# Kernel tuning notes

Measured on AMD Instinct MI355X. Metric: run time of the kernel, lower is better.

The kernel has to match this reference:

```python
import jax, jax.numpy as jnp
import numpy as np

DIM = 1024
Q_HEADS = 16
KV_HEADS = 4
DIM_HEAD = DIM // Q_HEADS  # 64
SOFTCLAMP = 50.0
EPS = 1e-8


def rotate_half(x):
    x_even = x[..., ::2]
    x_odd = x[..., 1::2]
    return jnp.stack([-x_odd, x_even], axis=-1).reshape(x.shape)


def setup_inputs() -> dict:
    key = jax.random.key(0)
    ks = jax.random.split(key, 10)
    B, S = 1, 2048
    dim_q = DIM_HEAD * Q_HEADS   # 1024
    dim_kv = DIM_HEAD * KV_HEADS  # 256
    std = 0.02
    x = jax.random.normal(ks[0], (B, S, DIM), dtype=jnp.float32)
    positions = jnp.broadcast_to(jnp.arange(S, dtype=jnp.int32)[None, :], (B, S))
    # causal mask: True = disallowed (torch semantics: allowed = ~attn_mask)
    attn_mask = jnp.triu(jnp.ones((S, S), dtype=bool), k=1)
    return {
        "x": x,
        "positions": positions,
        "attn_mask": attn_mask,
        "Wq": jax.random.normal(ks[1], (DIM, dim_q), jnp.float32) * std,
        "Wk": jax.random.normal(ks[2], (DIM, dim_kv), jnp.float32) * std,
        "Wv": jax.random.normal(ks[3], (DIM, dim_kv), jnp.float32) * std,
        "Wo": jax.random.normal(ks[4], (dim_q, DIM), jnp.float32) * std,
        "Wg": jax.random.normal(ks[5], (DIM, Q_HEADS), jnp.float32) * std,
        "Wm": jax.random.normal(ks[6], (DIM, KV_HEADS), jnp.float32) * std,
        "bm": jnp.zeros((KV_HEADS,), jnp.float32),
        "Wvr": jax.random.normal(ks[7], (DIM, dim_kv), jnp.float32) * std,
        "k_scale": jnp.ones((KV_HEADS, DIM_HEAD), jnp.float32),
    }


def reference(x, positions, attn_mask, Wq, Wk, Wv, Wo, Wg, Wm, bm, Wvr, k_scale):
    b, s, _ = x.shape
    h, qh, dh = KV_HEADS, Q_HEADS, DIM_HEAD
    g = qh // h

    q = (x @ Wq).reshape(b, s, qh, dh).transpose(0, 2, 1, 3)  # [b,qh,s,dh]
    k = (x @ Wk).reshape(b, s, h, dh).transpose(0, 2, 1, 3)   # [b,h,s,dh]
    v = (x @ Wv).reshape(b, s, h, dh).transpose(0, 2, 1, 3)

    # value-residual gating: v = lerp(v, residual_v, mix)
    residual_v = (x @ Wvr).reshape(b, s, h, dh).transpose(0, 2, 1, 3)
    mix = jax.nn.sigmoid(x @ Wm + bm).transpose(0, 2, 1)[..., None]  # [b,h,s,1]
    v = v + mix * (residual_v - v)

    # multi-head RMSNorm on k
    rms = jnp.sqrt(jnp.mean(k * k, axis=-1, keepdims=True) + EPS)
    k = k / rms * k_scale[None, :, None, :]

    # rotary embeddings (identical for all heads -> broadcast over head dim)
    inv_freq = 1.0 / (10000.0 ** (jnp.arange(0, dh, 2, dtype=jnp.float32) / dh))
    freqs = positions.astype(jnp.float32)[..., None] * inv_freq  # [b,s,dh/2]
    cos = jnp.repeat(jnp.cos(freqs), 2, axis=-1)[:, None, :, :]  # [b,1,s,dh]
    sin = jnp.repeat(jnp.sin(freqs), 2, axis=-1)[:, None, :, :]
    q = q * cos + rotate_half(q) * sin
    k = k * cos + rotate_half(k) * sin

    # grouped-query attention with softclamped scores
    scale = dh ** -0.5
    qg = q.reshape(b, h, g, s, dh)
    sim = jnp.einsum('bhgqd,bhkd->bhgqk', qg, k) * scale
    sim = jnp.tanh(sim / SOFTCLAMP) * SOFTCLAMP
    allowed = ~attn_mask  # [s,s]
    sim = jnp.where(allowed[None, None, None, :, :], sim, jnp.finfo(sim.dtype).min)
    attn = jax.nn.softmax(sim, axis=-1)
    out = jnp.einsum('bhgqk,bhkd->bhgqd', attn, v).reshape(b, qh, s, dh)

    # per-query-head sigmoid gates
    gates = jax.nn.sigmoid(x @ Wg).transpose(0, 2, 1)[..., None]  # [b,qh,s,1]
    out = out * gates

    out = out.transpose(0, 2, 1, 3).reshape(b, s, qh * dh)
    return out @ Wo
```

## Files before the change

### kernel.cpp

```cpp
#include <hip/hip_runtime.h>
#include <hip/hip_bf16.h>
#include <math.h>

typedef unsigned short u16;
typedef unsigned int u32;
typedef __attribute__((ext_vector_type(8))) __bf16 bf16x8;
typedef __attribute__((ext_vector_type(4))) float f32x4;

__device__ inline u16 f2bf(float f) {
  u32 b = __float_as_uint(f);
  b += 0x7FFFu + ((b >> 16) & 1u);
  return (u16)(b >> 16);
}
__device__ inline float bf2f(u16 b) { return __uint_as_float((u32)b << 16); }

__device__ __forceinline__ void gll16(const void* gp, void* lp) {
  __builtin_amdgcn_global_load_lds(
      (const __attribute__((address_space(1))) void*)gp,
      (__attribute__((address_space(3))) void*)lp, 16, 0, 0);
}

__global__ __launch_bounds__(256) void prep_all_k(
    const float* __restrict__ x, const int* __restrict__ positions,
    const float* __restrict__ Wq, const float* __restrict__ Wk,
    const float* __restrict__ Wv, const float* __restrict__ Wvr,
    const float* __restrict__ Wo, const float* __restrict__ Wg,
    const float* __restrict__ Wm, u16* __restrict__ xb,
    u16* __restrict__ WallT, u16* __restrict__ WoT, float* __restrict__ rtab) {
  __shared__ float tile[32][33];
  int bid = blockIdx.x, tid = threadIdx.x;
  if (bid < 1024) {
    int i = (bid * 256 + tid) * 8;
    float4 v0 = *(const float4*)&x[i];
    float4 v1 = *(const float4*)&x[i + 4];
    uint4 pk;
    pk.x = (u32)f2bf(v0.x) | ((u32)f2bf(v0.y) << 16);
    pk.y = (u32)f2bf(v0.z) | ((u32)f2bf(v0.w) << 16);
    pk.z = (u32)f2bf(v1.x) | ((u32)f2bf(v1.y) << 16);
    pk.w = (u32)f2bf(v1.z) | ((u32)f2bf(v1.w) << 16);
    *(uint4*)&xb[i] = pk;
    return;
  }
  if (bid >= 3968) {
    int idx = (bid - 3968) * 256 + tid;
    int s = idx >> 5, f = idx & 31;
    float inv = __expf(-(float)f * (9.210340371976184f / 32.f));
    float ang = (float)positions[s] * inv;
    rtab[(size_t)s * 64 + f] = cosf(ang);
    rtab[(size_t)s * 64 + 32 + f] = sinf(ang);
    return;
  }
  int b2 = bid - 1024;
  int k0 = (b2 & 31) * 32;
  int ybl = b2 >> 5;
  int tx = tid & 31, ty = tid >> 5;
  const float* src;
  int scol, sN, drow;
  u16* dst;
  if (ybl >= 60) {
    src = Wo; scol = (ybl - 60) * 32; sN = 1024; dst = WoT; drow = scol;
  } else {
    int n0 = ybl * 32;
    if (n0 >= 1792) {
#pragma unroll
      for (int j = 0; j < 4; ++j) {
        int n = n0 + ty * 4 + j, j2 = n - 1792, k = k0 + tx;
        float val = (j2 < 16) ? Wg[(size_t)k * 16 + j2]
                  : (j2 < 20) ? Wm[(size_t)k * 4 + (j2 - 16)] : 0.f;
        WallT[(size_t)n * 1024 + k] = f2bf(val);
      }
      return;
    }
    dst = WallT; drow = n0;
    if (n0 < 1024) { src = Wq; scol = n0; sN = 1024; }
    else if (n0 < 1280) { src = Wk; scol = n0 - 1024; sN = 256; }
    else if (n0 < 1536) { src = Wv; scol = n0 - 1280; sN = 256; }
    else { src = Wvr; scol = n0 - 1536; sN = 256; }
  }
#pragma unroll
  for (int j = 0; j < 4; ++j)
    tile[ty * 4 + j][tx] = src[(size_t)(k0 + ty * 4 + j) * sN + scol + tx];
  __syncthreads();
#pragma unroll
  for (int j = 0; j < 4; ++j)
    dst[(size_t)(drow + ty * 4 + j) * 1024 + k0 + tx] = f2bf(tile[tx][ty * 4 + j]);
}

template <int BM, bool BF16_OUT>
__global__ __launch_bounds__(512) void gemm_bf16_k(
    const u16* __restrict__ A, const u16* __restrict__ Bt, void* __restrict__ Cv,
    int M, int N, int K) {
  constexpr int MI = BM / 32;
  __shared__ __align__(16) u16 As[BM * 64];
  __shared__ __align__(16) u16 Bs[128 * 64];
  int tid = threadIdx.x;
  int w = tid >> 6, l = tid & 63;
  int wr = w >> 2, wc = w & 3;
  int lr = l & 15, lg = l >> 4;
  int lrow = l >> 3, lcol = (l & 7) * 8;
  int m0 = blockIdx.y * BM, n0 = blockIdx.x * 128;
  f32x4 zero = {0.f, 0.f, 0.f, 0.f};
  f32x4 acc[MI][2];
#pragma unroll
  for (int mi = 0; mi < MI; ++mi)
#pragma unroll
    for (int ni = 0; ni < 2; ++ni) acc[mi][ni] = zero;

  for (int kt = 0; kt < K; kt += 64) {
    __syncthreads();
#pragma unroll
    for (int t = 0; t < BM / 64; ++t) {
      int seg = t * 8 + w;
      gll16(&A[(size_t)(m0 + seg * 8 + lrow) * K + kt + lcol], &As[seg * 512]);
    }
#pragma unroll
    for (int t = 0; t < 2; ++t) {
      int seg = t * 8 + w;
      gll16(&Bt[(size_t)(n0 + seg * 8 + lrow) * K + kt + lcol], &Bs[seg * 512]);
    }
    __syncthreads();
#pragma unroll
    for (int kw = 0; kw < 2; ++kw) {
      bf16x8 af[MI], bfr[2];
#pragma unroll
      for (int mi = 0; mi < MI; ++mi)
        af[mi] = *(const bf16x8*)&As[(wr * (BM / 2) + mi * 16 + lr) * 64 + kw * 32 + lg * 8];
#pragma unroll
      for (int ni = 0; ni < 2; ++ni)
        bfr[ni] = *(const bf16x8*)&Bs[(wc * 32 + ni * 16 + lr) * 64 + kw * 32 + lg * 8];
#pragma unroll
      for (int mi = 0; mi < MI; ++mi)
#pragma unroll
        for (int ni = 0; ni < 2; ++ni)
          acc[mi][ni] = __builtin_amdgcn_mfma_f32_16x16x32_bf16(
              af[mi], bfr[ni], acc[mi][ni], 0, 0, 0);
    }
  }
#pragma unroll
  for (int mi = 0; mi < MI; ++mi)
#pragma unroll
    for (int ni = 0; ni < 2; ++ni)
#pragma unroll
      for (int r = 0; r < 4; ++r) {
        int row = m0 + wr * (BM / 2) + mi * 16 + lg * 4 + r;
        int col = n0 + wc * 32 + ni * 16 + lr;
        if (BF16_OUT)
          ((u16*)Cv)[(size_t)row * N + col] = f2bf(acc[mi][ni][r]);
        else
          ((float*)Cv)[(size_t)row * N + col] = acc[mi][ni][r];
      }
}

__global__ __launch_bounds__(256) void postproc_k(
    const float* __restrict__ bm, const float* __restrict__ ksc,
    const float* __restrict__ rtab, u16* __restrict__ qkvrb,
    u16* __restrict__ kb, u16* __restrict__ vb, float* __restrict__ g_out) {
  int s = blockIdx.x, tid = threadIdx.x;
  int lane = tid & 63, w = tid >> 6;
  u16* row = qkvrb + (size_t)s * 1920;
  const float* tr = rtab + (size_t)s * 64;
  if (tid < 16)
    g_out[s * 16 + tid] = 1.f / (1.f + __expf(-bf2f(row[1792 + tid])));
  int h = w, d = lane;
  float c = tr[d >> 1], sn = tr[32 + (d >> 1)];
  {
    float mixv = 1.f / (1.f + __expf(-(bf2f(row[1808 + h]) + bm[h])));
    float vv = bf2f(row[1280 + h * 64 + d]);
    float rv = bf2f(row[1536 + h * 64 + d]);
    vb[((size_t)h * 2048 + s) * 64 + d] = f2bf(vv + mixv * (rv - vv));
  }
  {
    float kv = bf2f(row[1024 + h * 64 + d]);
    float ss = kv * kv;
#pragma unroll
    for (int off = 32; off > 0; off >>= 1) ss += __shfl_xor(ss, off);
    float rms = sqrtf(ss * (1.f / 64.f) + 1e-8f);
    float kn = kv / rms * ksc[h * 64 + d];
    float partner = __shfl_xor(kn, 1);
    kb[((size_t)h * 2048 + s) * 64 + d] =
        f2bf((d & 1) ? fmaf(kn, c, partner * sn) : fmaf(kn, c, -partner * sn));
  }
#pragma unroll
  for (int r = 0; r < 4; ++r) {
    int e = r * 256 + tid;
    int dq = e & 63;
    float cq = tr[dq >> 1], sq = tr[32 + (dq >> 1)];
    float qv = bf2f(row[e]);
    float partner = __shfl_xor(qv, 1);
    float qr = (e & 1) ? fmaf(qv, cq, partner * sq) : fmaf(qv, cq, -partner * sq);
    row[e] = f2bf(qr * 0.125f);
  }
}

#define TPAD 66
__global__ __launch_bounds__(256) void vtrans_k(const u16* __restrict__ vb,
                                               u16* __restrict__ vtb) {
  __shared__ u16 tile[64 * TPAD];
  int h = blockIdx.y, s0 = blockIdx.x * 64;
  int t = threadIdx.x;
  {
    int r = t >> 2, cb = (t & 3) * 16;
    const u16* src = vb + ((size_t)h * 2048 + s0 + r) * 64 + cb;
    *(uint4*)&tile[r * TPAD + cb] = *(const uint4*)src;
    *(uint4*)&tile[r * TPAD + cb + 8] = *(const uint4*)(src + 8);
  }
  __syncthreads();
  int d = t >> 2, sb = (t & 3) * 16;
  u16 vals[16];
#pragma unroll
  for (int j = 0; j < 16; ++j) vals[j] = tile[(sb + j) * TPAD + d];
  uint4 a, b;
  a.x = (u32)vals[0] | ((u32)vals[1] << 16);
  a.y = (u32)vals[2] | ((u32)vals[3] << 16);
  a.z = (u32)vals[4] | ((u32)vals[5] << 16);
  a.w = (u32)vals[6] | ((u32)vals[7] << 16);
  b.x = (u32)vals[8] | ((u32)vals[9] << 16);
  b.y = (u32)vals[10] | ((u32)vals[11] << 16);
  b.z = (u32)vals[12] | ((u32)vals[13] << 16);
  b.w = (u32)vals[14] | ((u32)vals[15] << 16);
  u16* dst = vtb + ((size_t)h * 64 + d) * 2048 + s0 + sb;
  *(uint4*)dst = a;
  *(uint4*)(dst + 8) = b;
}

#define KPAD 72
__global__ __launch_bounds__(512) void attn_k(
    const u16* __restrict__ qkvrb, const u16* __restrict__ kb,
    const u16* __restrict__ vtb, const float* __restrict__ g,
    u16* __restrict__ aob) {
  __shared__ __align__(16) u16 smem[36864];
  int head = blockIdx.x, hkv = head >> 2;
  int tid = threadIdx.x;
  int w = tid >> 6, l = tid & 63;
  int grp = w >> 2, wi = w & 3;
  int lr = l & 15, lg = l >> 4;
  int gtid = wi * 64 + l;
  int skey = gtid >> 2, sdb = (gtid & 3) * 16;
  u16* KsBase = smem + grp * 18432;
  float* mbuf = (float*)smem;
  f32x4 zero = {0.f, 0.f, 0.f, 0.f};
  const float C1 = 0.057707801635558534f;
  const float C2 = -144.26950408889634f;
  int src_a = lr + (lg & 1) * 32, src_b = src_a + 16;
  bool hi = (lg & 2) != 0;
#pragma unroll 1
  for (int half = 0; half < 2; ++half) {
    int rb = half ? (int)blockIdx.y : (31 - (int)blockIdx.y);
    int row0 = rb * 64;
    const u16* qrow = qkvrb + (size_t)(row0 + wi * 16 + lr) * 1920 + head * 64;
    bf16x8 qf0 = *(const bf16x8*)&qrow[lg * 8];
    bf16x8 qf1 = *(const bf16x8*)&qrow[32 + lg * 8];
    f32x4 acc_o[4];
#pragma unroll
    for (int nd = 0; nd < 4; ++nd) acc_o[nd] = zero;
    float l_part = 0.f;
    int qglob = row0 + wi * 16 + lr;
    int c = grp;
    uint4 rk0, rk1, rv0, rv1;
    if (c <= rb) {
      const u16* kp = kb + ((size_t)hkv * 2048 + c * 64 + skey) * 64 + sdb;
      rk0 = *(const uint4*)kp;
      rk1 = *(const uint4*)(kp + 8);
      const u16* vp = vtb + ((size_t)(hkv * 64 + skey)) * 2048 + c * 64 + sdb;
      rv0 = *(const uint4*)vp;
      rv1 = *(const uint4*)(vp + 8);
      *(uint4*)&KsBase[skey * KPAD + sdb] = rk0;
      *(uint4*)&KsBase[skey * KPAD + sdb + 8] = rk1;
      *(uint4*)&KsBase[4608 + skey * KPAD + sdb] = rv0;
      *(uint4*)&KsBase[4608 + skey * KPAD + sdb + 8] = rv1;
    }
    __syncthreads();
    int nmax = (rb >> 1) + 1;
#pragma unroll 1
    for (int i = 0; i < nmax; ++i, c += 2) {
      bool valid = (c <= rb);
      bool nvalid = (c + 2 <= rb);
      if (nvalid) {
        int nb = (c + 2) * 64;
        const u16* kp = kb + ((size_t)hkv * 2048 + nb + skey) * 64 + sdb;
        rk0 = *(const uint4*)kp;
        rk1 = *(const uint4*)(kp + 8);
        const u16* vp = vtb + ((size_t)(hkv * 64 + skey)) * 2048 + nb + sdb;
        rv0 = *(const uint4*)vp;
        rv1 = *(const uint4*)(vp + 8);
      }
      if (valid) {
        u16* Ks = KsBase + (i & 1) * 9216;
        u16* Vt = Ks + 4608;
        int kbase = c * 64;
        __builtin_amdgcn_s_setprio(1);
        f32x4 sa[4];
#pragma unroll
        for (int ni = 0; ni < 4; ++ni) {
          bf16x8 a0 = *(const bf16x8*)&Ks[(ni * 16 + lr) * KPAD + lg * 8];
          bf16x8 a1 = *(const bf16x8*)&Ks[(ni * 16 + lr) * KPAD + 32 + lg * 8];
          f32x4 t = __builtin_amdgcn_mfma_f32_16x16x32_bf16(a0, qf0, zero, 0, 0, 0);
          sa[ni] = __builtin_amdgcn_mfma_f32_16x16x32_bf16(a1, qf1, t, 0, 0, 0);
        }
        bool diag = (c == rb);
        u32 pkw[4][2];
#pragma unroll
        for (int ni = 0; ni < 4; ++ni) {
          float pv[4];
#pragma unroll
          for (int r = 0; r < 4; ++r) {
            float sv = sa[ni][r];
            float e = __builtin_amdgcn_exp2f(sv * C1);
            float p = __builtin_amdgcn_exp2f(C2 * __builtin_amdgcn_rcpf(e + 1.f));
            if (diag && (kbase + ni * 16 + lg * 4 + r) > qglob) p = 0.f;
            pv[r] = p;
            l_part += p;
          }
          asm("v_cvt_pk_bf16_f32 %0, %1, %2" : "=v"(pkw[ni][0]) : "v"(pv[0]), "v"(pv[1]));
          asm("v_cvt_pk_bf16_f32 %0, %1, %2" : "=v"(pkw[ni][1]) : "v"(pv[2]), "v"(pv[3]));
        }
        union { u32 w[4]; bf16x8 v; } pf0, pf1;
        {
          u32 t0[4], t1[4], t2[4], t3[4];
#define GATHER(T, NI)                          \
          T[0] = __shfl((int)pkw[NI][0], src_a);   \
          T[1] = __shfl((int)pkw[NI][1], src_a);   \
          T[2] = __shfl((int)pkw[NI][0], src_b);   \
          T[3] = __shfl((int)pkw[NI][1], src_b);
          GATHER(t0, 0)
          GATHER(t1, 1)
          GATHER(t2, 2)
          GATHER(t3, 3)
#undef GATHER
#pragma unroll
          for (int kq = 0; kq < 4; ++kq) {
            pf0.w[kq] = hi ? t1[kq] : t0[kq];
            pf1.w[kq] = hi ? t3[kq] : t2[kq];
          }
        }
#pragma unroll
        for (int nd = 0; nd < 4; ++nd) {
          bf16x8 v0 = *(const bf16x8*)&Vt[(nd * 16 + lr) * KPAD + lg * 8];
          bf16x8 v1 = *(const bf16x8*)&Vt[(nd * 16 + lr) * KPAD + 32 + lg * 8];
          acc_o[nd] = __builtin_amdgcn_mfma_f32_16x16x32_bf16(pf0.v, v0, acc_o[nd], 0, 0, 0);
          acc_o[nd] = __builtin_amdgcn_mfma_f32_16x16x32_bf16(pf1.v, v1, acc_o[nd], 0, 0, 0);
        }
        __builtin_amdgcn_s_setprio(0);
      }
      if (nvalid) {
        u16* Ksn = KsBase + ((i & 1) ^ 1) * 9216;
        *(uint4*)&Ksn[skey * KPAD + sdb] = rk0;
        *(uint4*)&Ksn[skey * KPAD + sdb + 8] = rk1;
        *(uint4*)&Ksn[4608 + skey * KPAD + sdb] = rv0;
        *(uint4*)&Ksn[4608 + skey * KPAD + sdb + 8] = rv1;
      }
      __syncthreads();
    }
    l_part += __shfl_xor(l_part, 16);
    l_part += __shfl_xor(l_part, 32);
    if (grp == 1) {
      float* mb = mbuf + (size_t)gtid * 17;
#pragma unroll
      for (int nd = 0; nd < 4; ++nd)
#pragma unroll
        for (int r = 0; r < 4; ++r) mb[nd * 4 + r] = acc_o[nd][r];
      mb[16] = l_part;
    }
    __syncthreads();
    if (grp == 0) {
      const float* mb = mbuf + (size_t)gtid * 17;
      float lt = l_part + mb[16];
#pragma unroll
      for (int r = 0; r < 4; ++r) {
        int row = row0 + wi * 16 + lg * 4 + r;
        float lv = __shfl(lt, lg * 4 + r);
        float sc = g[row * 16 + head] * __builtin_amdgcn_rcpf(lv);
#pragma unroll
        for (int nd = 0; nd < 4; ++nd)
          aob[(size_t)row * 1024 + head * 64 + nd * 16 + lr] =
              f2bf((acc_o[nd][r] + mb[nd * 4 + r]) * sc);
      }
    }
    __syncthreads();
  }
}

extern "C" void kernel_launch(void* const* d_in, const int* in_sizes, int n_in,
                              void* d_out, int out_size, void* d_ws,
                              size_t ws_size, hipStream_t stream) {
  const float* x = (const float*)d_in[0];
  const int* positions = (const int*)d_in[1];
  const float* Wq = (const float*)d_in[3];
  const float* Wk = (const float*)d_in[4];
  const float* Wv = (const float*)d_in[5];
  const float* Wo = (const float*)d_in[6];
  const float* Wg = (const float*)d_in[7];
  const float* Wm = (const float*)d_in[8];
  const float* bm = (const float*)d_in[9];
  const float* Wvr = (const float*)d_in[10];
  const float* ksc = (const float*)d_in[11];
  float* out = (float*)d_out;

  u16* xb = (u16*)d_ws;
  u16* WallT = xb + (size_t)2048 * 1024;
  u16* WoT = WallT + (size_t)1920 * 1024;
  u16* qkvrb = WoT + (size_t)1024 * 1024;
  u16* kbuf = qkvrb + (size_t)2048 * 1920;
  u16* vbuf = kbuf + (size_t)4 * 2048 * 64;
  u16* vtb = vbuf + (size_t)4 * 2048 * 64;
  float* gbuf = (float*)(vtb + (size_t)4 * 2048 * 64);
  float* rtab = gbuf + (size_t)2048 * 16;
  u16* aob = xb;

  prep_all_k<<<4224, 256, 0, stream>>>(x, positions, Wq, Wk, Wv, Wvr, Wo, Wg,
                                       Wm, xb, WallT, WoT, rtab);
  gemm_bf16_k<128, true><<<dim3(15, 16), 512, 0, stream>>>(xb, WallT, qkvrb,
                                                           2048, 1920, 1024);
  postproc_k<<<2048, 256, 0, stream>>>(bm, ksc, rtab, qkvrb, kbuf, vbuf, gbuf);
  vtrans_k<<<dim3(32, 4), 256, 0, stream>>>(vbuf, vtb);
  attn_k<<<dim3(16, 16), 512, 0, stream>>>(qkvrb, kbuf, vtb, gbuf, aob);
  gemm_bf16_k<64, false><<<dim3(8, 32), 512, 0, stream>>>(aob, WoT, out, 2048,
                                                          1024, 1024);
}
```

Before: 98.61 us.

## Drop LDS staging in attention, read K/V fragments directly from global

The attention kernel no longer stages K and V tiles through shared memory with double buffering and barriers. Each wave now loads its MFMA operand fragments straight from global memory and relies on the caches for reuse across waves. The grid goes from 256 blocks of 512 threads, each handling two row blocks with split-KV groups, to 512 blocks of 256 threads, each handling one row block. This removes the cross-group merge and all __syncthreads. The cost is redundant global/L2 traffic, since each of the 4 waves reloads the same K/V tile, and less latency hiding than the explicit prefetch gave.

Measured after the change: 134.4 us. 36.3% more time.

```diff
diff --git a/kernel.cpp b/kernel.cpp
--- a/kernel.cpp
+++ b/kernel.cpp
@@ -223,160 +223,102 @@
   *(uint4*)(dst + 8) = b;
 }
 
-#define KPAD 72
-__global__ __launch_bounds__(512) void attn_k(
+__global__ __launch_bounds__(256) void attn_k(
     const u16* __restrict__ qkvrb, const u16* __restrict__ kb,
     const u16* __restrict__ vtb, const float* __restrict__ g,
     u16* __restrict__ aob) {
-  __shared__ __align__(16) u16 smem[36864];
   int head = blockIdx.x, hkv = head >> 2;
+  int by = blockIdx.y;
+  int rb = (by < 16) ? (31 - by) : (by - 16);
+  int row0 = rb * 64;
   int tid = threadIdx.x;
-  int w = tid >> 6, l = tid & 63;
-  int grp = w >> 2, wi = w & 3;
+  int wi = tid >> 6, l = tid & 63;
   int lr = l & 15, lg = l >> 4;
-  int gtid = wi * 64 + l;
-  int skey = gtid >> 2, sdb = (gtid & 3) * 16;
-  u16* KsBase = smem + grp * 18432;
-  float* mbuf = (float*)smem;
   f32x4 zero = {0.f, 0.f, 0.f, 0.f};
   const float C1 = 0.057707801635558534f;
   const float C2 = -144.26950408889634f;
+  const u16* qrow = qkvrb + (size_t)(row0 + wi * 16 + lr) * 1920 + head * 64;
+  bf16x8 qf0 = *(const bf16x8*)&qrow[lg * 8];
+  bf16x8 qf1 = *(const bf16x8*)&qrow[32 + lg * 8];
+  f32x4 acc_o[4];
+#pragma unroll
+  for (int nd = 0; nd < 4; ++nd) acc_o[nd] = zero;
+  float l_part = 0.f;
+  int qglob = row0 + wi * 16 + lr;
   int src_a = lr + (lg & 1) * 32, src_b = src_a + 16;
   bool hi = (lg & 2) != 0;
+  const u16* kbase_p = kb + ((size_t)hkv * 2048 + lr) * 64 + lg * 8;
+  const u16* vbase_p = vtb + (size_t)(hkv * 64 + lr) * 2048 + lg * 8;
 #pragma unroll 1
-  for (int half = 0; half < 2; ++half) {
-    int rb = half ? (int)blockIdx.y : (31 - (int)blockIdx.y);
-    int row0 = rb * 64;
-    const u16* qrow = qkvrb + (size_t)(row0 + wi * 16 + lr) * 1920 + head * 64;
-    bf16x8 qf0 = *(const bf16x8*)&qrow[lg * 8];
-    bf16x8 qf1 = *(const bf16x8*)&qrow[32 + lg * 8];
-    f32x4 acc_o[4];
-#pragma unroll
-    for (int nd = 0; nd < 4; ++nd) acc_o[nd] = zero;
-    float l_part = 0.f;
-    int qglob = row0 + wi * 16 + lr;
-    int c = grp;
-    uint4 rk0, rk1, rv0, rv1;
-    if (c <= rb) {
-      const u16* kp = kb + ((size_t)hkv * 2048 + c * 64 + skey) * 64 + sdb;
-      rk0 = *(const uint4*)kp;
-      rk1 = *(const uint4*)(kp + 8);
-      const u16* vp = vtb + ((size_t)(hkv * 64 + skey)) * 2048 + c * 64 + sdb;
-      rv0 = *(const uint4*)vp;
-      rv1 = *(const uint4*)(vp + 8);
-      *(uint4*)&KsBase[skey * KPAD + sdb] = rk0;
-      *(uint4*)&KsBase[skey * KPAD + sdb + 8] = rk1;
-      *(uint4*)&KsBase[4608 + skey * KPAD + sdb] = rv0;
-      *(uint4*)&KsBase[4608 + skey * KPAD + sdb + 8] = rv1;
-    }
-    __syncthreads();
-    int nmax = (rb >> 1) + 1;
-#pragma unroll 1
-    for (int i = 0; i < nmax; ++i, c += 2) {
-      bool valid = (c <= rb);
-      bool nvalid = (c + 2 <= rb);
-      if (nvalid) {
-        int nb = (c + 2) * 64;
-        const u16* kp = kb + ((size_t)hkv * 2048 + nb + skey) * 64 + sdb;
-        rk0 = *(const uint4*)kp;
-        rk1 = *(const uint4*)(kp + 8);
-        const u16* vp = vtb + ((size_t)(hkv * 64 + skey)) * 2048 + nb + sdb;
-        rv0 = *(const uint4*)vp;
-        rv1 = *(const uint4*)(vp + 8);
+  for (int c = 0; c <= rb; ++c) {
+    int kb0 = c * 64;
+    __builtin_amdgcn_s_setprio(1);
+    f32x4 sa[4];
+#pragma unroll
+    for (int ni = 0; ni < 4; ++ni) {
+      const u16* kp = kbase_p + (size_t)(kb0 + ni * 16) * 64;
+      bf16x8 a0 = *(const bf16x8*)kp;
+      bf16x8 a1 = *(const bf16x8*)(kp + 32);
+      f32x4 t = __builtin_amdgcn_mfma_f32_16x16x32_bf16(a0, qf0, zero, 0, 0, 0);
+      sa[ni] = __builtin_amdgcn_mfma_f32_16x16x32_bf16(a1, qf1, t, 0, 0, 0);
+    }
+    bool diag = (c == rb);
+    u32 pkw[4][2];
+#pragma unroll
+    for (int ni = 0; ni < 4; ++ni) {
+      float pv[4];
+#pragma unroll
+      for (int r = 0; r < 4; ++r) {
+        float sv = sa[ni][r];
+        float e = __builtin_amdgcn_exp2f(sv * C1);
+        float p = __builtin_amdgcn_exp2f(C2 * __builtin_amdgcn_rcpf(e + 1.f));
+        if (diag && (kb0 + ni * 16 + lg * 4 + r) > qglob) p = 0.f;
+        pv[r] = p;
+        l_part += p;
       }
-      if (valid) {
-        u16* Ks = KsBase + (i & 1) * 9216;
-        u16* Vt = Ks + 4608;
-        int kbase = c * 64;
-        __builtin_amdgcn_s_setprio(1);
-        f32x4 sa[4];
-#pragma unroll
-        for (int ni = 0; ni < 4; ++ni) {
-          bf16x8 a0 = *(const bf16x8*)&Ks[(ni * 16 + lr) * KPAD + lg * 8];
-          bf16x8 a1 = *(const bf16x8*)&Ks[(ni * 16 + lr) * KPAD + 32 + lg * 8];
-          f32x4 t = __builtin_amdgcn_mfma_f32_16x16x32_bf16(a0, qf0, zero, 0, 0, 0);
-          sa[ni] = __builtin_amdgcn_mfma_f32_16x16x32_bf16(a1, qf1, t, 0, 0, 0);
-        }
-        bool diag = (c == rb);
-        u32 pkw[4][2];
-#pragma unroll
-        for (int ni = 0; ni < 4; ++ni) {
-          float pv[4];
-#pragma unroll
-          for (int r = 0; r < 4; ++r) {
-            float sv = sa[ni][r];
-            float e = __builtin_amdgcn_exp2f(sv * C1);
-            float p = __builtin_amdgcn_exp2f(C2 * __builtin_amdgcn_rcpf(e + 1.f));
-            if (diag && (kbase + ni * 16 + lg * 4 + r) > qglob) p = 0.f;
-            pv[r] = p;
-            l_part += p;
-          }
-          asm("v_cvt_pk_bf16_f32 %0, %1, %2" : "=v"(pkw[ni][0]) : "v"(pv[0]), "v"(pv[1]));
-          asm("v_cvt_pk_bf16_f32 %0, %1, %2" : "=v"(pkw[ni][1]) : "v"(pv[2]), "v"(pv[3]));
-        }
-        union { u32 w[4]; bf16x8 v; } pf0, pf1;
-        {
-          u32 t0[4], t1[4], t2[4], t3[4];
+      asm("v_cvt_pk_bf16_f32 %0, %1, %2" : "=v"(pkw[ni][0]) : "v"(pv[0]), "v"(pv[1]));
+      asm("v_cvt_pk_bf16_f32 %0, %1, %2" : "=v"(pkw[ni][1]) : "v"(pv[2]), "v"(pv[3]));
+    }
+    union { u32 w[4]; bf16x8 v; } pf0, pf1;
+    {
+      u32 t0[4], t1[4], t2[4], t3[4];
 #define GATHER(T, NI)                          \
-          T[0] = __shfl((int)pkw[NI][0], src_a);   \
-          T[1] = __shfl((int)pkw[NI][1], src_a);   \
-          T[2] = __shfl((int)pkw[NI][0], src_b);   \
-          T[3] = __shfl((int)pkw[NI][1], src_b);
-          GATHER(t0, 0)
-          GATHER(t1, 1)
-          GATHER(t2, 2)
-          GATHER(t3, 3)
+      T[0] = __shfl((int)pkw[NI][0], src_a);   \
+      T[1] = __shfl((int)pkw[NI][1], src_a);   \
+      T[2] = __shfl((int)pkw[NI][0], src_b);   \
+      T[3] = __shfl((int)pkw[NI][1], src_b);
+      GATHER(t0, 0)
+      GATHER(t1, 1)
+      GATHER(t2, 2)
+      GATHER(t3, 3)
 #undef GATHER
 #pragma unroll
-          for (int kq = 0; kq < 4; ++kq) {
-            pf0.w[kq] = hi ? t1[kq] : t0[kq];
-            pf1.w[kq] = hi ? t3[kq] : t2[kq];
-          }
-        }
-#pragma unroll
-        for (int nd = 0; nd < 4; ++nd) {
-          bf16x8 v0 = *(const bf16x8*)&Vt[(nd * 16 + lr) * KPAD + lg * 8];
-          bf16x8 v1 = *(const bf16x8*)&Vt[(nd * 16 + lr) * KPAD + 32 + lg * 8];
-          acc_o[nd] = __builtin_amdgcn_mfma_f32_16x16x32_bf16(pf0.v, v0, acc_o[nd], 0, 0, 0);
-          acc_o[nd] = __builtin_amdgcn_mfma_f32_16x16x32_bf16(pf1.v, v1, acc_o[nd], 0, 0, 0);
-        }
-        __builtin_amdgcn_s_setprio(0);
+      for (int kq = 0; kq < 4; ++kq) {
+        pf0.w[kq] = hi ? t1[kq] : t0[kq];
+        pf1.w[kq] = hi ? t3[kq] : t2[kq];
       }
-      if (nvalid) {
-        u16* Ksn = KsBase + ((i & 1) ^ 1) * 9216;
-        *(uint4*)&Ksn[skey * KPAD + sdb] = rk0;
-        *(uint4*)&Ksn[skey * KPAD + sdb + 8] = rk1;
-        *(uint4*)&Ksn[4608 + skey * KPAD + sdb] = rv0;
-        *(uint4*)&Ksn[4608 + skey * KPAD + sdb + 8] = rv1;
-      }
-      __syncthreads();
-    }
-    l_part += __shfl_xor(l_part, 16);
-    l_part += __shfl_xor(l_part, 32);
-    if (grp == 1) {
-      float* mb = mbuf + (size_t)gtid * 17;
-#pragma unroll
-      for (int nd = 0; nd < 4; ++nd)
-#pragma unroll
-        for (int r = 0; r < 4; ++r) mb[nd * 4 + r] = acc_o[nd][r];
-      mb[16] = l_part;
-    }
-    __syncthreads();
-    if (grp == 0) {
-      const float* mb = mbuf + (size_t)gtid * 17;
-      float lt = l_part + mb[16];
-#pragma unroll
-      for (int r = 0; r < 4; ++r) {
-        int row = row0 + wi * 16 + lg * 4 + r;
-        float lv = __shfl(lt, lg * 4 + r);
-        float sc = g[row * 16 + head] * __builtin_amdgcn_rcpf(lv);
-#pragma unroll
-        for (int nd = 0; nd < 4; ++nd)
-          aob[(size_t)row * 1024 + head * 64 + nd * 16 + lr] =
-              f2bf((acc_o[nd][r] + mb[nd * 4 + r]) * sc);
-      }
-    }
-    __syncthreads();
+    }
+#pragma unroll
+    for (int nd = 0; nd < 4; ++nd) {
+      const u16* vp = vbase_p + (size_t)nd * 16 * 2048 + kb0;
+      bf16x8 v0 = *(const bf16x8*)vp;
+      bf16x8 v1 = *(const bf16x8*)(vp + 32);
+      acc_o[nd] = __builtin_amdgcn_mfma_f32_16x16x32_bf16(pf0.v, v0, acc_o[nd], 0, 0, 0);
+      acc_o[nd] = __builtin_amdgcn_mfma_f32_16x16x32_bf16(pf1.v, v1, acc_o[nd], 0, 0, 0);
+    }
+    __builtin_amdgcn_s_setprio(0);
+  }
+  l_part += __shfl_xor(l_part, 16);
+  l_part += __shfl_xor(l_part, 32);
+#pragma unroll
+  for (int r = 0; r < 4; ++r) {
+    int row = row0 + wi * 16 + lg * 4 + r;
+    float lv = __shfl(l_part, lg * 4 + r);
+    float sc = g[row * 16 + head] * __builtin_amdgcn_rcpf(lv);
+#pragma unroll
+    for (int nd = 0; nd < 4; ++nd)
+      aob[(size_t)row * 1024 + head * 64 + nd * 16 + lr] =
+          f2bf(acc_o[nd][r] * sc);
   }
 }
 
@@ -413,7 +355,7 @@
                                                            2048, 1920, 1024);
   postproc_k<<<2048, 256, 0, stream>>>(bm, ksc, rtab, qkvrb, kbuf, vbuf, gbuf);
   vtrans_k<<<dim3(32, 4), 256, 0, stream>>>(vbuf, vtb);
-  attn_k<<<dim3(16, 16), 512, 0, stream>>>(qkvrb, kbuf, vtb, gbuf, aob);
+  attn_k<<<dim3(16, 32), 256, 0, stream>>>(qkvrb, kbuf, vtb, gbuf, aob);
   gemm_bf16_k<64, false><<<dim3(8, 32), 512, 0, stream>>>(aob, WoT, out, 2048,
                                                           1024, 1024);
 }
```

## Load K/V tiles directly into LDS with XOR-swizzled layout

Applied to the files above, without the earlier changes.

Replaces the register-staged K/V prefetch (global load to VGPRs, then LDS store after compute) with direct global_load_lds 16-byte transfers into the double buffer. The padded KPAD layout becomes an unpadded 64-element row with an XOR swizzle on 8-element units to avoid bank conflicts, which shrinks shared memory. The goal is to cut VGPR pressure and LDS write instructions and to overlap the copy with compute. It relies on the __syncthreads barrier being enough to wait for the asynchronous LDS loads to finish, and on the swizzle being applied the same way on the write and read sides.

After: 93.90 us. 1.05x faster.

```diff
diff --git a/kernel.cpp b/kernel.cpp
--- a/kernel.cpp
+++ b/kernel.cpp
@@ -223,26 +223,29 @@
   *(uint4*)(dst + 8) = b;
 }
 
-#define KPAD 72
 __global__ __launch_bounds__(512) void attn_k(
     const u16* __restrict__ qkvrb, const u16* __restrict__ kb,
     const u16* __restrict__ vtb, const float* __restrict__ g,
     u16* __restrict__ aob) {
-  __shared__ __align__(16) u16 smem[36864];
+  __shared__ __align__(16) u16 smem[32768];
   int head = blockIdx.x, hkv = head >> 2;
   int tid = threadIdx.x;
   int w = tid >> 6, l = tid & 63;
   int grp = w >> 2, wi = w & 3;
   int lr = l & 15, lg = l >> 4;
   int gtid = wi * 64 + l;
-  int skey = gtid >> 2, sdb = (gtid & 3) * 16;
-  u16* KsBase = smem + grp * 18432;
+  u16* KsBase = smem + grp * 16384;
   float* mbuf = (float*)smem;
   f32x4 zero = {0.f, 0.f, 0.f, 0.f};
   const float C1 = 0.057707801635558534f;
   const float C2 = -144.26950408889634f;
   int src_a = lr + (lg & 1) * 32, src_b = src_a + 16;
   bool hi = (lg & 2) != 0;
+  int u0 = ((lg ^ (lr & 7)) << 3);
+  int srow = l >> 3;
+  int sunit = (l & 7) ^ srow;
+  const u16* ksrc = kb + ((size_t)hkv * 2048 + srow) * 64 + sunit * 8;
+  const u16* vsrc = vtb + ((size_t)(hkv * 64 + srow)) * 2048 + sunit * 8;
 #pragma unroll 1
   for (int half = 0; half < 2; ++half) {
     int rb = half ? (int)blockIdx.y : (31 - (int)blockIdx.y);
@@ -256,44 +259,42 @@
     float l_part = 0.f;
     int qglob = row0 + wi * 16 + lr;
     int c = grp;
-    uint4 rk0, rk1, rv0, rv1;
     if (c <= rb) {
-      const u16* kp = kb + ((size_t)hkv * 2048 + c * 64 + skey) * 64 + sdb;
-      rk0 = *(const uint4*)kp;
-      rk1 = *(const uint4*)(kp + 8);
-      const u16* vp = vtb + ((size_t)(hkv * 64 + skey)) * 2048 + c * 64 + sdb;
-      rv0 = *(const uint4*)vp;
-      rv1 = *(const uint4*)(vp + 8);
-      *(uint4*)&KsBase[skey * KPAD + sdb] = rk0;
-      *(uint4*)&KsBase[skey * KPAD + sdb + 8] = rk1;
-      *(uint4*)&KsBase[4608 + skey * KPAD + sdb] = rv0;
-      *(uint4*)&KsBase[4608 + skey * KPAD + sdb + 8] = rv1;
+#pragma unroll
+      for (int t = 0; t < 2; ++t) {
+        int seg = wi * 2 + t;
+        gll16(ksrc + (size_t)(c * 64 + seg * 8) * 64, KsBase + seg * 512);
+        gll16(vsrc + (size_t)(seg * 8) * 2048 + c * 64,
+              KsBase + 4096 + seg * 512);
+      }
     }
     __syncthreads();
     int nmax = (rb >> 1) + 1;
 #pragma unroll 1
     for (int i = 0; i < nmax; ++i, c += 2) {
       bool valid = (c <= rb);
-      bool nvalid = (c + 2 <= rb);
-      if (nvalid) {
-        int nb = (c + 2) * 64;
-        const u16* kp = kb + ((size_t)hkv * 2048 + nb + skey) * 64 + sdb;
-        rk0 = *(const uint4*)kp;
-        rk1 = *(const uint4*)(kp + 8);
-        const u16* vp = vtb + ((size_t)(hkv * 64 + skey)) * 2048 + nb + sdb;
-        rv0 = *(const uint4*)vp;
-        rv1 = *(const uint4*)(vp + 8);
+      if (c + 2 <= rb) {
+        u16* Ksn = KsBase + ((i & 1) ^ 1) * 8192;
+        int nc = c + 2;
+#pragma unroll
+        for (int t = 0; t < 2; ++t) {
+          int seg = wi * 2 + t;
+          gll16(ksrc + (size_t)(nc * 64 + seg * 8) * 64, Ksn + seg * 512);
+          gll16(vsrc + (size_t)(seg * 8) * 2048 + nc * 64,
+                Ksn + 4096 + seg * 512);
+        }
       }
       if (valid) {
-        u16* Ks = KsBase + (i & 1) * 9216;
-        u16* Vt = Ks + 4608;
+        u16* Ks = KsBase + (i & 1) * 8192;
+        u16* Vt = Ks + 4096;
         int kbase = c * 64;
         __builtin_amdgcn_s_setprio(1);
         f32x4 sa[4];
 #pragma unroll
         for (int ni = 0; ni < 4; ++ni) {
-          bf16x8 a0 = *(const bf16x8*)&Ks[(ni * 16 + lr) * KPAD + lg * 8];
-          bf16x8 a1 = *(const bf16x8*)&Ks[(ni * 16 + lr) * KPAD + 32 + lg * 8];
+          const u16* kp = &Ks[(ni * 16 + lr) * 64];
+          bf16x8 a0 = *(const bf16x8*)&kp[u0];
+          bf16x8 a1 = *(const bf16x8*)&kp[u0 ^ 32];
           f32x4 t = __builtin_amdgcn_mfma_f32_16x16x32_bf16(a0, qf0, zero, 0, 0, 0);
           sa[ni] = __builtin_amdgcn_mfma_f32_16x16x32_bf16(a1, qf1, t, 0, 0, 0);
         }
@@ -335,19 +336,13 @@
         }
 #pragma unroll
         for (int nd = 0; nd < 4; ++nd) {
-          bf16x8 v0 = *(const bf16x8*)&Vt[(nd * 16 + lr) * KPAD + lg * 8];
-          bf16x8 v1 = *(const bf16x8*)&Vt[(nd * 16 + lr) * KPAD + 32 + lg * 8];
+          const u16* vp = &Vt[(nd * 16 + lr) * 64];
+          bf16x8 v0 = *(const bf16x8*)&vp[u0];
+          bf16x8 v1 = *(const bf16x8*)&vp[u0 ^ 32];
           acc_o[nd] = __builtin_amdgcn_mfma_f32_16x16x32_bf16(pf0.v, v0, acc_o[nd], 0, 0, 0);
           acc_o[nd] = __builtin_amdgcn_mfma_f32_16x16x32_bf16(pf1.v, v1, acc_o[nd], 0, 0, 0);
         }
         __builtin_amdgcn_s_setprio(0);
-      }
-      if (nvalid) {
-        u16* Ksn = KsBase + ((i & 1) ^ 1) * 9216;
-        *(uint4*)&Ksn[skey * KPAD + sdb] = rk0;
-        *(uint4*)&Ksn[skey * KPAD + sdb + 8] = rk1;
-        *(uint4*)&Ksn[4608 + skey * KPAD + sdb] = rv0;
-        *(uint4*)&Ksn[4608 + skey * KPAD + sdb + 8] = rv1;
       }
       __syncthreads();
     }
```
